# Kernel optimization log

Measured on AMD Instinct MI355X. Metric: run time of the kernel, lower is better.

## Reference

```python
import jax, jax.numpy as jnp
import numpy as np

B, N, M, C = 4, 2048, 576, 512
H, KVH, D = 8, 2, 64          # heads, kv heads, head_dim
E, TOPK, F = 8, 2, 2048       # experts, top-k, expert hidden (4*C)
EPS = 1e-6
NEG = -1e9


def setup_inputs() -> dict:
    key = jax.random.key(0)
    ks = iter(jax.random.split(key, 40))
    w = lambda shape, s=0.02: jax.random.normal(next(ks), shape, jnp.float32) * s
    d = {
        'x': jax.random.normal(next(ks), (B, N, C), jnp.float32),
        'vision_features': jax.random.normal(next(ks), (B, M, C), jnp.float32),
        'ln1_g': jnp.ones((C,), jnp.float32), 'ln1_b': jnp.zeros((C,), jnp.float32),
        'ln2_g': jnp.ones((C,), jnp.float32), 'ln2_b': jnp.zeros((C,), jnp.float32),
        'ln3_g': jnp.ones((C,), jnp.float32), 'ln3_b': jnp.zeros((C,), jnp.float32),
        # self-attention (GQA): q -> C, k/v -> KVH*D
        'sa_wq': w((C, C)), 'sa_bq': jnp.zeros((C,), jnp.float32),
        'sa_wk': w((C, KVH * D)), 'sa_bk': jnp.zeros((KVH * D,), jnp.float32),
        'sa_wv': w((C, KVH * D)), 'sa_bv': jnp.zeros((KVH * D,), jnp.float32),
        'sa_wo': w((C, C)), 'sa_bo': jnp.zeros((C,), jnp.float32),
        # cross-attention (GQA)
        'ca_wq': w((C, C)), 'ca_bq': jnp.zeros((C,), jnp.float32),
        'ca_wk': w((C, KVH * D)), 'ca_bk': jnp.zeros((KVH * D,), jnp.float32),
        'ca_wv': w((C, KVH * D)), 'ca_bv': jnp.zeros((KVH * D,), jnp.float32),
        'ca_wo': w((C, C)), 'ca_bo': jnp.zeros((C,), jnp.float32),
        # MoE: router + stacked expert MLPs (C -> F -> C, GELU)
        'router_w': w((C, E)), 'router_b': jnp.zeros((E,), jnp.float32),
        'e_w1': w((E, C, F)), 'e_b1': jnp.zeros((E, F), jnp.float32),
        'e_w2': w((E, F, C)), 'e_b2': jnp.zeros((E, C), jnp.float32),
    }
    return d


def _ln(x, g, b):
    mu = jnp.mean(x, -1, keepdims=True)
    var = jnp.mean(jnp.square(x - mu), -1, keepdims=True)
    return (x - mu) * jax.lax.rsqrt(var + EPS) * g + b


def _gqa_attn(xq, ctx, wq, bq, wk, bk, wv, bv, wo, bo, causal):
    b, n, c = xq.shape
    m = ctx.shape[1]
    q = (xq @ wq + bq).reshape(b, n, H, D).transpose(0, 2, 1, 3)      # bhnd
    k = (ctx @ wk + bk).reshape(b, m, KVH, D).transpose(0, 2, 1, 3)   # bgmd
    v = (ctx @ wv + bv).reshape(b, m, KVH, D).transpose(0, 2, 1, 3)
    rep = H // KVH
    k = jnp.repeat(k, rep, axis=1)  # repeat_interleave over head dim
    v = jnp.repeat(v, rep, axis=1)
    scores = jnp.einsum('bhnd,bhmd->bhnm', q, k) * (D ** -0.5)
    if causal:
        mask = jnp.tril(jnp.ones((n, m), bool))
        scores = jnp.where(mask, scores, NEG)
    a = jax.nn.softmax(scores, axis=-1)
    o = jnp.einsum('bhnm,bhmd->bhnd', a, v).transpose(0, 2, 1, 3).reshape(b, n, c)
    return o @ wo + bo


def _moe(x, router_w, router_b, e_w1, e_b1, e_w2, e_b2):
    logits = x @ router_w + router_b                    # [B,N,E]
    probs = jax.nn.softmax(logits, axis=-1)
    topv, topi = jax.lax.top_k(probs, TOPK)             # [B,N,K]
    topv = topv / jnp.sum(topv, -1, keepdims=True)      # renormalize top-k gates
    onehot = jax.nn.one_hot(topi, E, dtype=x.dtype)     # [B,N,K,E]
    gates = jnp.einsum('bnke,bnk->bne', onehot, topv)   # sparse gates, zeros off top-k
    h = jax.nn.gelu(jnp.einsum('bnc,ecf->bnef', x, e_w1) + e_b1)
    eo = jnp.einsum('bnef,efc->bnec', h, e_w2) + e_b2
    out = jnp.einsum('bne,bnec->bnc', gates, eo)
    # load-balance aux loss (Switch-style): E * sum_e f_e * P_e
    dispatch = jnp.sum(onehot, axis=2)                  # [B,N,E] routed mask
    f = jnp.mean(dispatch, axis=(0, 1))
    P = jnp.mean(probs, axis=(0, 1))
    aux = E * jnp.sum(f * P)
    return out, aux


def reference(x, vision_features,
              ln1_g, ln1_b, ln2_g, ln2_b, ln3_g, ln3_b,
              sa_wq, sa_bq, sa_wk, sa_bk, sa_wv, sa_bv, sa_wo, sa_bo,
              ca_wq, ca_bq, ca_wk, ca_bk, ca_wv, ca_bv, ca_wo, ca_bo,
              router_w, router_b, e_w1, e_b1, e_w2, e_b2):
    # pre-norm causal self-attn + residual
    h = _ln(x, ln1_g, ln1_b)
    x = x + _gqa_attn(h, h, sa_wq, sa_bq, sa_wk, sa_bk, sa_wv, sa_bv, sa_wo, sa_bo, True)
    # pre-norm cross-attn + residual
    h = _ln(x, ln2_g, ln2_b)
    x = x + _gqa_attn(h, vision_features, ca_wq, ca_bq, ca_wk, ca_bk, ca_wv, ca_bv, ca_wo, ca_bo, False)
    # pre-norm MoE FFN + residual
    h = _ln(x, ln3_g, ln3_b)
    m, aux = _moe(h, router_w, router_b, e_w1, e_b1, e_w2, e_b2)
    return x + m, aux
```

## Files before the change

kernel.cpp:

```cpp
#include <hip/hip_runtime.h>
#include <cstddef>
#include <cstdint>

#define B_   4
#define N_   2048
#define M_   576
#define C_   512
#define H_   8
#define KVH_ 2
#define D_   64
#define E_   8
#define F_   2048
#define BN_  (B_*N_)
#define BM_  (B_*M_)

typedef __attribute__((ext_vector_type(8))) short bf16x8;
typedef __attribute__((ext_vector_type(4))) float f32x4;

__device__ __forceinline__ unsigned short f2bf(float f) {
    union { float f; unsigned int u; } v; v.f = f;
    unsigned int r = v.u + 0x7FFFu + ((v.u >> 16) & 1u);
    return (unsigned short)(r >> 16);
}
__device__ __forceinline__ float bf2f(unsigned short u) {
    union { unsigned int u; float f; } v; v.u = ((unsigned int)u) << 16;
    return v.f;
}

typedef __attribute__((address_space(1))) void glb_void;
typedef __attribute__((address_space(3))) void lds_void;
__device__ __forceinline__ void gl2lds16(const unsigned short* g, unsigned short* l) {
    __builtin_amdgcn_global_load_lds((glb_void*)g, (lds_void*)l, 16, 0, 0);
}

__global__ __launch_bounds__(256) void prep_all(
    const float* __restrict__ sa_wq, const float* __restrict__ sa_wk,
    const float* __restrict__ sa_wv, const float* __restrict__ sa_wo,
    const float* __restrict__ ca_wq, const float* __restrict__ ca_wk,
    const float* __restrict__ ca_wv, const float* __restrict__ ca_wo,
    const float* __restrict__ e_w1, const float* __restrict__ e_w2,
    const float* __restrict__ vis,
    const float* __restrict__ sa_bk, const float* __restrict__ sa_bv,
    const float* __restrict__ ca_bk, const float* __restrict__ ca_bv,
    unsigned short* __restrict__ sa_wqt, unsigned short* __restrict__ sa_wkvt,
    unsigned short* __restrict__ sa_wot,
    unsigned short* __restrict__ ca_wqt, unsigned short* __restrict__ ca_wkvt,
    unsigned short* __restrict__ ca_wot,
    unsigned short* __restrict__ w1t, unsigned short* __restrict__ w2t,
    unsigned short* __restrict__ visbf,
    float* __restrict__ bkv_sa, float* __restrict__ bkv_ca,
    int* __restrict__ ctrl)
{
    __shared__ float T[32][33];
    int t = blockIdx.x;
    int tid = threadIdx.x;

    if (t < 17664) {
        const float* W; unsigned short* Wt; int K, N, kt, nt;
        if (t < 1280) {
            if (t < 256)      { W = sa_wq; Wt = sa_wqt; K = 512; N = 512; int r = t;        nt = r & 15; kt = r >> 4; }
            else if (t < 320) { W = sa_wk; Wt = sa_wkvt;            K = 512; N = 128; int r = t - 256; nt = r & 3;  kt = r >> 2; }
            else if (t < 384) { W = sa_wv; Wt = sa_wkvt + 128*512;  K = 512; N = 128; int r = t - 320; nt = r & 3;  kt = r >> 2; }
            else if (t < 640) { W = sa_wo; Wt = sa_wot; K = 512; N = 512; int r = t - 384;  nt = r & 15; kt = r >> 4; }
            else if (t < 896) { W = ca_wq; Wt = ca_wqt; K = 512; N = 512; int r = t - 640;  nt = r & 15; kt = r >> 4; }
            else if (t < 960) { W = ca_wk; Wt = ca_wkvt;            K = 512; N = 128; int r = t - 896; nt = r & 3;  kt = r >> 2; }
            else if (t < 1024){ W = ca_wv; Wt = ca_wkvt + 128*512;  K = 512; N = 128; int r = t - 960; nt = r & 3;  kt = r >> 2; }
            else              { W = ca_wo; Wt = ca_wot; K = 512; N = 512; int r = t - 1024; nt = r & 15; kt = r >> 4; }
        } else if (t < 9472) {
            int r = t - 1280; int e = r >> 10; r &= 1023;
            W = e_w1 + (size_t)e * C_ * F_; Wt = w1t + (size_t)e * C_ * F_;
            K = C_; N = F_; nt = r & 63; kt = r >> 6;
        } else {
            int r = t - 9472; int e = r >> 10; r &= 1023;
            W = e_w2 + (size_t)e * F_ * C_; Wt = w2t + (size_t)e * F_ * C_;
            K = F_; N = C_; nt = r & 15; kt = r >> 4;
        }
        int rr = tid >> 3, c4 = (tid & 7) * 4;
        int k0 = kt * 32, n0 = nt * 32;
        float4 v = *(const float4*)&W[(size_t)(k0 + rr) * N + n0 + c4];
        T[rr][c4 + 0] = v.x; T[rr][c4 + 1] = v.y; T[rr][c4 + 2] = v.z; T[rr][c4 + 3] = v.w;
        __syncthreads();
        ushort4 o;
        o.x = f2bf(T[c4 + 0][rr]); o.y = f2bf(T[c4 + 1][rr]);
        o.z = f2bf(T[c4 + 2][rr]); o.w = f2bf(T[c4 + 3][rr]);
        *(ushort4*)&Wt[(size_t)(n0 + rr) * K + k0 + c4] = o;
    } else if (t < 18816) {
        int i = (t - 17664) * 1024 + tid * 4;
        float4 v = *(const float4*)(vis + i);
        ushort4 o;
        o.x = f2bf(v.x); o.y = f2bf(v.y); o.z = f2bf(v.z); o.w = f2bf(v.w);
        *(ushort4*)(visbf + i) = o;
    } else {
        if (tid < 128) {
            bkv_sa[tid]       = sa_bk[tid];
            bkv_sa[128 + tid] = sa_bv[tid];
            bkv_ca[tid]       = ca_bk[tid];
            bkv_ca[128 + tid] = ca_bv[tid];
        }
        if (tid < 32) ctrl[tid] = 0;
    }
}

__global__ __launch_bounds__(256) void ln_bf(const float* __restrict__ x,
    const float* __restrict__ g, const float* __restrict__ b, unsigned short* __restrict__ out)
{
    int row = blockIdx.x;
    const float* xr = x + (size_t)row * C_;
    float s = 0.f, ss = 0.f;
    for (int c = threadIdx.x; c < C_; c += 256) { float v = xr[c]; s += v; ss += v * v; }
    __shared__ float S1[256], S2[256];
    S1[threadIdx.x] = s; S2[threadIdx.x] = ss;
    __syncthreads();
    for (int o = 128; o > 0; o >>= 1) {
        if (threadIdx.x < o) { S1[threadIdx.x] += S1[threadIdx.x + o]; S2[threadIdx.x] += S2[threadIdx.x + o]; }
        __syncthreads();
    }
    float mu  = S1[0] * (1.f / C_);
    float var = S2[0] * (1.f / C_) - mu * mu;
    float inv = rsqrtf(var + 1e-6f);
    unsigned short* orow = out + (size_t)row * C_;
    for (int c = threadIdx.x; c < C_; c += 256)
        orow[c] = f2bf((xr[c] - mu) * inv * g[c] + b[c]);
}

__global__ __launch_bounds__(256) void ln_dual(const float* __restrict__ x,
    const float* __restrict__ g, const float* __restrict__ b,
    float* __restrict__ outF, unsigned short* __restrict__ outBf)
{
    int row = blockIdx.x;
    const float* xr = x + (size_t)row * C_;
    float s = 0.f, ss = 0.f;
    for (int c = threadIdx.x; c < C_; c += 256) { float v = xr[c]; s += v; ss += v * v; }
    __shared__ float S1[256], S2[256];
    S1[threadIdx.x] = s; S2[threadIdx.x] = ss;
    __syncthreads();
    for (int o = 128; o > 0; o >>= 1) {
        if (threadIdx.x < o) { S1[threadIdx.x] += S1[threadIdx.x + o]; S2[threadIdx.x] += S2[threadIdx.x + o]; }
        __syncthreads();
    }
    float mu  = S1[0] * (1.f / C_);
    float var = S2[0] * (1.f / C_) - mu * mu;
    float inv = rsqrtf(var + 1e-6f);
    for (int c = threadIdx.x; c < C_; c += 256) {
        float v = (xr[c] - mu) * inv * g[c] + b[c];
        outF[(size_t)row * C_ + c] = v;
        outBf[(size_t)row * C_ + c] = f2bf(v);
    }
}

__global__ __launch_bounds__(256) void dense_mfma(
    const unsigned short* __restrict__ Abf,
    const unsigned short* __restrict__ Btbf,
    const float* __restrict__ bias,
    const float* __restrict__ xin,
    float* __restrict__ outF,
    unsigned short* __restrict__ outBf,
    unsigned short* __restrict__ outBf2,
    int N, int K, int mode, int NkPer)
{
    int row0 = blockIdx.y * 128;
    int col0 = blockIdx.x * 128;

    __shared__ unsigned short As[128 * 32];
    __shared__ unsigned short Bs[128 * 32];

    int tid = threadIdx.x;
    int lane = tid & 63, wid = tid >> 6;
    int lrow = lane >> 2;
    int cswz = (((lane & 3) ^ ((lane >> 3) & 3)) << 3);
    int ar0 = 16 * (wid * 2) + lrow;
    int ar1 = ar0 + 16;
    const unsigned short* gA0 = Abf + (size_t)(row0 + ar0) * K + cswz;
    const unsigned short* gA1 = Abf + (size_t)(row0 + ar1) * K + cswz;
    const unsigned short* gB0 = Btbf + (size_t)(col0 + ar0) * K + cswz;
    const unsigned short* gB1 = Btbf + (size_t)(col0 + ar1) * K + cswz;
    unsigned short* lA0 = As + (wid * 2) * 512;
    unsigned short* lA1 = lA0 + 512;
    unsigned short* lB0 = Bs + (wid * 2) * 512;
    unsigned short* lB1 = lB0 + 512;

    int wm0 = (wid & 1) * 64, wn0 = (wid >> 1) * 64;
    int lm = lane & 15, lq = lane >> 4;
    int swb = (lq ^ ((lm >> 1) & 3)) << 3;
    int aoff[4], boff[4];
#pragma unroll
    for (int i = 0; i < 4; i++) {
        aoff[i] = (wm0 + 16 * i + lm) * 32 + swb;
        boff[i] = (wn0 + 16 * i + lm) * 32 + swb;
    }

    f32x4 acc[4][4];
#pragma unroll
    for (int i = 0; i < 4; i++)
#pragma unroll
        for (int j = 0; j < 4; j++)
            acc[i][j] = (f32x4){0.f, 0.f, 0.f, 0.f};

    for (int k0 = 0; k0 < K; k0 += 32) {
        __syncthreads();
        gl2lds16(gA0 + k0, lA0);
        gl2lds16(gA1 + k0, lA1);
        gl2lds16(gB0 + k0, lB0);
        gl2lds16(gB1 + k0, lB1);
        __syncthreads();

        bf16x8 av[4], bv[4];
#pragma unroll
        for (int i = 0; i < 4; i++) av[i] = *(const bf16x8*)&As[aoff[i]];
#pragma unroll
        for (int i = 0; i < 4; i++) bv[i] = *(const bf16x8*)&Bs[boff[i]];
#pragma unroll
        for (int mi = 0; mi < 4; mi++)
#pragma unroll
            for (int ni = 0; ni < 4; ni++)
                acc[mi][ni] = __builtin_amdgcn_mfma_f32_16x16x32_bf16(av[mi], bv[ni], acc[mi][ni], 0, 0, 0);
    }

#pragma unroll
    for (int mi = 0; mi < 4; mi++) {
#pragma unroll
        for (int ri = 0; ri < 4; ri++) {
            int gr = row0 + wm0 + 16 * mi + lq * 4 + ri;
            if (mode == 3) {
#pragma unroll
                for (int ni = 0; ni < 4; ni++) {
                    int gc = col0 + wn0 + 16 * ni + lm;
                    float v = acc[mi][ni][ri] + bias[gc];
                    if (gc < 128) {
                        outBf[(size_t)gr * 128 + gc] = f2bf(v);
                    } else {
                        int bb = gr / NkPer;
                        int mm = gr - bb * NkPer;
                        outBf2[((size_t)bb * 128 + (gc - 128)) * NkPer + mm] = f2bf(v);
                    }
                }
            } else if (mode == 1) {
                size_t orow = (size_t)gr * N;
#pragma unroll
                for (int ni = 0; ni < 4; ni++) {
                    int gc = col0 + wn0 + 16 * ni + lm;
                    outF[orow + gc] += acc[mi][ni][ri] + bias[gc];
                }
            } else if (mode == 4) {
                size_t orow = (size_t)gr * N;
#pragma unroll
                for (int ni = 0; ni < 4; ni++) {
                    int gc = col0 + wn0 + 16 * ni + lm;
                    outF[orow + gc] = xin[orow + gc] + acc[mi][ni][ri] + bias[gc];
                }
            } else {
                size_t orow = (size_t)gr * N;
#pragma unroll
                for (int ni = 0; ni < 4; ni++) {
                    int gc = col0 + wn0 + 16 * ni + lm;
                    outBf[orow + gc] = f2bf(acc[mi][ni][ri] + bias[gc]);
                }
            }
        }
    }
}

__global__ __launch_bounds__(256) void attn_mfma(
    const unsigned short* __restrict__ Q,
    const unsigned short* __restrict__ K,
    const unsigned short* __restrict__ Vt,
    unsigned short* __restrict__ Obf,
    float* __restrict__ Opart,
    float* __restrict__ Lpart,
    int NkPer, int causal)
{
    __shared__ unsigned short Qs[64 * 72];
    __shared__ unsigned short Ks[64 * 72];
    __shared__ unsigned short Vs[64 * 72];
    unsigned short* Ps = Qs;

    int tid = threadIdx.x;
    int qt = blockIdx.x, bh = blockIdx.y, z = blockIdx.z;
    int b = bh >> 3, h = bh & 7, g = h >> 2;
    int q0 = qt * 64;

#pragma unroll
    for (int i = 0; i < 2; i++) {
        int s = tid + (i << 8);
        int r = s >> 3, c8 = (s & 7) << 3;
        *(uint4*)&Qs[r * 72 + c8] =
            *(const uint4*)&Q[(size_t)(b * N_ + q0 + r) * C_ + h * D_ + c8];
    }
    __syncthreads();

    int lane = tid & 63, wid = tid >> 6;
    int lm = lane & 15, lq = lane >> 4;
    int arow = wid * 16 + lm;

    bf16x8 qf[2];
    qf[0] = *(const bf16x8*)&Qs[arow * 72 + lq * 8];
    qf[1] = *(const bf16x8*)&Qs[arow * 72 + lq * 8 + 32];

    float lsum[4];
    f32x4 of[4];
#pragma unroll
    for (int i = 0; i < 4; i++) { lsum[i] = 0.f; of[i] = (f32x4){0.f,0.f,0.f,0.f}; }

    int nkt = causal ? (qt + 1) : ((NkPer + 63) >> 6);
    int nz = gridDim.z;
    int per = (nkt + nz - 1) / nz;
    int kt0 = z * per;
    int kt1 = min(nkt, kt0 + per);

    for (int kt = kt0; kt < kt1; kt++) {
        int k0 = kt << 6;
        __syncthreads();
#pragma unroll
        for (int i = 0; i < 2; i++) {
            int s = tid + (i << 8);
            int r = s >> 3, c8 = (s & 7) << 3;
            *(uint4*)&Ks[r * 72 + c8] =
                *(const uint4*)&K[(size_t)(b * NkPer + k0 + r) * (KVH_ * D_) + g * D_ + c8];
            *(uint4*)&Vs[r * 72 + c8] =
                *(const uint4*)&Vt[(size_t)(b * (KVH_ * D_) + g * D_ + r) * NkPer + k0 + c8];
        }
        __syncthreads();

        f32x4 sf[4];
#pragma unroll
        for (int i = 0; i < 4; i++) sf[i] = (f32x4){0.f,0.f,0.f,0.f};
#pragma unroll
        for (int ks = 0; ks < 2; ks++) {
#pragma unroll
            for (int ni = 0; ni < 4; ni++) {
                bf16x8 bv = *(const bf16x8*)&Ks[(16 * ni + lm) * 72 + lq * 8 + 32 * ks];
                sf[ni] = __builtin_amdgcn_mfma_f32_16x16x32_bf16(qf[ks], bv, sf[ni], 0, 0, 0);
            }
        }

        bool diag = causal && (k0 + 63 > q0 + wid * 16);
#pragma unroll
        for (int ni = 0; ni < 4; ni++)
#pragma unroll
            for (int ri = 0; ri < 4; ri++) {
                float v = sf[ni][ri] * 0.125f - 8.f;
                if (diag && (k0 + 16 * ni + lm > q0 + wid * 16 + lq * 4 + ri)) v = -1e30f;
                float p = __expf(v);
                sf[ni][ri] = p;
                lsum[ri] += p;
            }

#pragma unroll
        for (int ni = 0; ni < 4; ni++)
#pragma unroll
            for (int ri = 0; ri < 4; ri++)
                Ps[(wid * 16 + lq * 4 + ri) * 72 + 16 * ni + lm] = f2bf(sf[ni][ri]);
        __syncthreads();

        bf16x8 pf0 = *(const bf16x8*)&Ps[arow * 72 + lq * 8];
        bf16x8 pf1 = *(const bf16x8*)&Ps[arow * 72 + lq * 8 + 32];
#pragma unroll
        for (int ni = 0; ni < 4; ni++) {
            bf16x8 vv0 = *(const bf16x8*)&Vs[(16 * ni + lm) * 72 + lq * 8];
            bf16x8 vv1 = *(const bf16x8*)&Vs[(16 * ni + lm) * 72 + lq * 8 + 32];
            of[ni] = __builtin_amdgcn_mfma_f32_16x16x32_bf16(pf0, vv0, of[ni], 0, 0, 0);
            of[ni] = __builtin_amdgcn_mfma_f32_16x16x32_bf16(pf1, vv1, of[ni], 0, 0, 0);
        }
    }

#pragma unroll
    for (int ri = 0; ri < 4; ri++) {
        float s = lsum[ri];
        s += __shfl_xor(s, 1);
        s += __shfl_xor(s, 2);
        s += __shfl_xor(s, 4);
        s += __shfl_xor(s, 8);
        lsum[ri] = s;
    }

    if (nz == 1) {
#pragma unroll
        for (int ri = 0; ri < 4; ri++) {
            float inv = 1.f / lsum[ri];
            int q = q0 + wid * 16 + lq * 4 + ri;
            size_t orow = (size_t)(b * N_ + q) * C_ + h * D_;
#pragma unroll
            for (int ni = 0; ni < 4; ni++)
                Obf[orow + 16 * ni + lm] = f2bf(of[ni][ri] * inv);
        }
    } else {
        size_t zofs = (size_t)z * BN_ * C_;
#pragma unroll
        for (int ri = 0; ri < 4; ri++) {
            int q = q0 + wid * 16 + lq * 4 + ri;
            size_t orow = zofs + (size_t)(b * N_ + q) * C_ + h * D_;
#pragma unroll
            for (int ni = 0; ni < 4; ni++)
                Opart[orow + 16 * ni + lm] = of[ni][ri];
            if (lm == 0)
                Lpart[(size_t)z * (B_ * H_ * N_) + bh * N_ + q] = lsum[ri];
        }
    }
}

__global__ __launch_bounds__(256) void attn_combine(const float* __restrict__ Opart,
    const float* __restrict__ Lpart, unsigned short* __restrict__ Obf)
{
    int flat = (blockIdx.x * 256 + threadIdx.x) * 4;
    int row = flat >> 9, col = flat & 511;
    int b = row >> 11, q = row & (N_ - 1), h = col >> 6;
    int bh = b * 8 + h;
    float l = Lpart[bh * N_ + q] + Lpart[B_ * H_ * N_ + bh * N_ + q];
    float inv = 1.f / l;
    float4 o0 = *(const float4*)&Opart[flat];
    float4 o1 = *(const float4*)&Opart[(size_t)BN_ * C_ + flat];
    ushort4 o;
    o.x = f2bf((o0.x + o1.x) * inv); o.y = f2bf((o0.y + o1.y) * inv);
    o.z = f2bf((o0.z + o1.z) * inv); o.w = f2bf((o0.w + o1.w) * inv);
    *(ushort4*)&Obf[flat] = o;
}

__global__ __launch_bounds__(256) void router_logits(const float* __restrict__ X,
    const float* __restrict__ RW, const float* __restrict__ RB,
    float* __restrict__ gprobs, int* __restrict__ topi, float* __restrict__ gatesv)
{
    int lane = threadIdx.x & 63;
    int t = blockIdx.x * 4 + (threadIdx.x >> 6);
    const float* xr = X + (size_t)t * C_;
    float p[8] = {};
    for (int i = 0; i < 8; i++) {
        int c = i * 64 + lane;
        float xv = xr[c];
#pragma unroll
        for (int e = 0; e < 8; e++) p[e] = fmaf(xv, RW[c * 8 + e], p[e]);
    }
#pragma unroll
    for (int e = 0; e < 8; e++) {
        float v = p[e];
        v += __shfl_xor(v, 32, 64);
        v += __shfl_xor(v, 16, 64);
        v += __shfl_xor(v, 8, 64);
        v += __shfl_xor(v, 4, 64);
        v += __shfl_xor(v, 2, 64);
        v += __shfl_xor(v, 1, 64);
        p[e] = v;
    }
    if (lane == 0) {
        float logits[8], mx = -1e30f;
        for (int e = 0; e < 8; e++) { logits[e] = p[e] + RB[e]; mx = fmaxf(mx, logits[e]); }
        float pr[8], sum = 0.f;
        for (int e = 0; e < 8; e++) { pr[e] = expf(logits[e] - mx); sum += pr[e]; }
        float inv = 1.f / sum;
        for (int e = 0; e < 8; e++) { pr[e] *= inv; gprobs[t * 8 + e] = pr[e]; }
        int i1 = 0;
        for (int e = 1; e < 8; e++) if (pr[e] > pr[i1]) i1 = e;
        int i2 = (i1 == 0) ? 1 : 0;
        for (int e = 0; e < 8; e++) if (e != i1 && pr[e] > pr[i2]) i2 = e;
        float v1 = pr[i1], v2 = pr[i2], sg = 1.f / (v1 + v2);
        topi[t * 2]     = i1;  topi[t * 2 + 1]   = i2;
        gatesv[t * 2]   = v1 * sg;  gatesv[t * 2 + 1] = v2 * sg;
    }
}

__global__ __launch_bounds__(256) void router_reduce(const float* __restrict__ gprobs,
    const int* __restrict__ topi, int* __restrict__ ctrl, float* __restrict__ psum)
{
    __shared__ float fs[256];
    __shared__ int   is_[256];
    int bid = blockIdx.x, tid = threadIdx.x;
    if (bid < 8) {
        float s = 0.f;
        for (int t = tid; t < BN_; t += 256) s += gprobs[t * 8 + bid];
        fs[tid] = s; __syncthreads();
        for (int o = 128; o > 0; o >>= 1) { if (tid < o) fs[tid] += fs[tid + o]; __syncthreads(); }
        if (tid == 0) psum[bid] = fs[0];
    } else {
        int e = bid - 8, c = 0;
        for (int i = tid; i < BN_ * 2; i += 256) c += (topi[i] == e);
        is_[tid] = c; __syncthreads();
        for (int o = 128; o > 0; o >>= 1) { if (tid < o) is_[tid] += is_[tid + o]; __syncthreads(); }
        if (tid == 0) ctrl[e] = is_[0];
    }
}

__global__ void router_offsets(int* __restrict__ ctrl)
{
    if (threadIdx.x == 0 && blockIdx.x == 0) {
        int off = 0;
        for (int e = 0; e < 8; e++) {
            ctrl[16 + e] = off;
            off += (ctrl[e] + 127) & ~127;
        }
        ctrl[24] = off;
    }
}

__global__ __launch_bounds__(256) void router_scatter(const int* __restrict__ topi,
    const float* __restrict__ gatesv, int* __restrict__ rowtok,
    int* __restrict__ slotidx, int* __restrict__ ctrl)
{
    __shared__ int lcnt[8];
    __shared__ int lbase[8];
    int tid = threadIdx.x;
    int t = blockIdx.x * 256 + tid;
    if (tid < 8) lcnt[tid] = 0;
    __syncthreads();
    int e0 = topi[t * 2], e1 = topi[t * 2 + 1];
    int p0 = atomicAdd(&lcnt[e0], 1);
    int p1 = atomicAdd(&lcnt[e1], 1);
    __syncthreads();
    if (tid < 8) lbase[tid] = atomicAdd(&ctrl[8 + tid], lcnt[tid]);
    __syncthreads();
    int s0 = ctrl[16 + e0] + lbase[e0] + p0;
    int s1 = ctrl[16 + e1] + lbase[e1] + p1;
    rowtok[s0] = t;
    rowtok[s1] = t;
    slotidx[t * 2]     = s0;
    slotidx[t * 2 + 1] = s1;
}

__global__ __launch_bounds__(256) void moe_mfma(
    const unsigned short* __restrict__ Abf,
    const unsigned short* __restrict__ Btbf,
    const float* __restrict__ biasAll,
    unsigned short* __restrict__ outBf,
    const int* __restrict__ rowtok,
    const int* __restrict__ ctrl,
    int N, int K, int mode)
{
    int e = blockIdx.z;
    int cnt = ctrl[e];
    int row0 = blockIdx.y * 128;
    if (row0 >= cnt) return;
    int off = ctrl[16 + e];
    int col0 = blockIdx.x * 128;
    const unsigned short* Bt = Btbf + (size_t)e * N * K;
    const float* bias = biasAll + (size_t)e * N;

    __shared__ unsigned short As[128 * 64];
    __shared__ unsigned short Bs[128 * 64];
    __shared__ int toks[128];

    int tid = threadIdx.x;
    if (mode == 1 && tid < 128) {
        int gl = row0 + tid;
        toks[tid] = rowtok[off + (gl < cnt ? gl : 0)];
    }
    __syncthreads();

    int lane = tid & 63, wid = tid >> 6;
    int r8 = lane >> 3;
    size_t asrc[4], bsrc[4];
    unsigned short *adst[4], *bdst[4];
#pragma unroll
    for (int i = 0; i < 4; i++) {
        int rA = wid * 32 + i * 8 + r8;
        int srcc = (((lane & 7) ^ (rA & 7)) << 3);
        size_t arow = (mode == 1) ? (size_t)toks[rA] * K
                                  : (size_t)(off + row0 + rA) * K;
        asrc[i] = arow + srcc;
        bsrc[i] = (size_t)(col0 + rA) * K + srcc;
        adst[i] = As + (wid * 32 + i * 8) * 64;
        bdst[i] = Bs + (wid * 32 + i * 8) * 64;
    }

    int wm0 = (wid & 1) * 64, wn0 = (wid >> 1) * 64;
    int lm = lane & 15, lq = lane >> 4;
    int x7 = lm & 7;
    int aoff[4][2], boff[4][2];
#pragma unroll
    for (int i = 0; i < 4; i++) {
#pragma unroll
        for (int ks = 0; ks < 2; ks++) {
            int swz = (((ks << 2) + lq) ^ x7) << 3;
            aoff[i][ks] = (wm0 + 16 * i + lm) * 64 + swz;
            boff[i][ks] = (wn0 + 16 * i + lm) * 64 + swz;
        }
    }

    f32x4 acc[4][4];
#pragma unroll
    for (int i = 0; i < 4; i++)
#pragma unroll
        for (int j = 0; j < 4; j++)
            acc[i][j] = (f32x4){0.f, 0.f, 0.f, 0.f};

    for (int k0 = 0; k0 < K; k0 += 64) {
        __syncthreads();
#pragma unroll
        for (int i = 0; i < 4; i++) {
            gl2lds16(Abf + asrc[i] + k0, adst[i]);
            gl2lds16(Bt  + bsrc[i] + k0, bdst[i]);
        }
        __syncthreads();

#pragma unroll
        for (int ks = 0; ks < 2; ks++) {
            bf16x8 av[4], bv[4];
#pragma unroll
            for (int i = 0; i < 4; i++) av[i] = *(const bf16x8*)&As[aoff[i][ks]];
#pragma unroll
            for (int i = 0; i < 4; i++) bv[i] = *(const bf16x8*)&Bs[boff[i][ks]];
#pragma unroll
            for (int mi = 0; mi < 4; mi++)
#pragma unroll
                for (int ni = 0; ni < 4; ni++)
                    acc[mi][ni] = __builtin_amdgcn_mfma_f32_16x16x32_bf16(av[mi], bv[ni], acc[mi][ni], 0, 0, 0);
        }
    }

#pragma unroll
    for (int mi = 0; mi < 4; mi++) {
#pragma unroll
        for (int ri = 0; ri < 4; ri++) {
            int gl = row0 + wm0 + 16 * mi + lq * 4 + ri;
            size_t orow = (size_t)(off + gl) * N;
            if (mode == 1) {
#pragma unroll
                for (int ni = 0; ni < 4; ni++) {
                    int gc = col0 + wn0 + 16 * ni + lm;
                    float hv = 0.f;
                    if (gl < cnt) {
                        float xv = acc[mi][ni][ri] + bias[gc];
                        float z = 0.7978845608f * xv * fmaf(0.044715f, xv * xv, 1.f);
                        hv = __fdividef(xv, 1.f + __expf(-2.f * z));
                    }
                    outBf[orow + gc] = f2bf(hv);
                }
            } else {
#pragma unroll
                for (int ni = 0; ni < 4; ni++) {
                    int gc = col0 + wn0 + 16 * ni + lm;
                    outBf[orow + gc] = f2bf(acc[mi][ni][ri] + bias[gc]);
                }
            }
        }
    }
}

__global__ __launch_bounds__(256) void moe_combine(const unsigned short* __restrict__ slots,
    const int* __restrict__ slotidx, const float* __restrict__ gatesv,
    float* __restrict__ out)
{
    int flat = (blockIdx.x * 256 + threadIdx.x) * 4;
    int t = flat >> 9, c = flat & 511;
    int s0 = slotidx[t * 2], s1 = slotidx[t * 2 + 1];
    float g0 = gatesv[t * 2], g1 = gatesv[t * 2 + 1];
    ushort4 a = *(const ushort4*)&slots[(size_t)s0 * C_ + c];
    ushort4 b = *(const ushort4*)&slots[(size_t)s1 * C_ + c];
    float4 o = *(float4*)&out[flat];
    o.x += g0 * bf2f(a.x) + g1 * bf2f(b.x);
    o.y += g0 * bf2f(a.y) + g1 * bf2f(b.y);
    o.z += g0 * bf2f(a.z) + g1 * bf2f(b.z);
    o.w += g0 * bf2f(a.w) + g1 * bf2f(b.w);
    *(float4*)&out[flat] = o;
}

__global__ void aux_kernel(const int* __restrict__ ctrl, const float* __restrict__ psum,
                           float* __restrict__ outaux)
{
    if (threadIdx.x == 0 && blockIdx.x == 0) {
        float s = 0.f;
        for (int e = 0; e < 8; e++)
            s += ((float)ctrl[e] / (float)BN_) * (psum[e] / (float)BN_);
        outaux[0] = 8.f * s;
    }
}

extern "C" void kernel_launch(void* const* d_in, const int* in_sizes, int n_in,
                              void* d_out, int out_size, void* d_ws, size_t ws_size,
                              hipStream_t stream)
{
    const float* x      = (const float*)d_in[0];
    const float* vis    = (const float*)d_in[1];
    const float* ln1g   = (const float*)d_in[2];
    const float* ln1b   = (const float*)d_in[3];
    const float* ln2g   = (const float*)d_in[4];
    const float* ln2b   = (const float*)d_in[5];
    const float* ln3g   = (const float*)d_in[6];
    const float* ln3b   = (const float*)d_in[7];
    const float* sa_wq  = (const float*)d_in[8];
    const float* sa_bq  = (const float*)d_in[9];
    const float* sa_wk  = (const float*)d_in[10];
    const float* sa_bk  = (const float*)d_in[11];
    const float* sa_wv  = (const float*)d_in[12];
    const float* sa_bv  = (const float*)d_in[13];
    const float* sa_wo  = (const float*)d_in[14];
    const float* sa_bo  = (const float*)d_in[15];
    const float* ca_wq  = (const float*)d_in[16];
    const float* ca_bq  = (const float*)d_in[17];
    const float* ca_wk  = (const float*)d_in[18];
    const float* ca_bk  = (const float*)d_in[19];
    const float* ca_wv  = (const float*)d_in[20];
    const float* ca_bv  = (const float*)d_in[21];
    const float* ca_wo  = (const float*)d_in[22];
    const float* ca_bo  = (const float*)d_in[23];
    const float* rw     = (const float*)d_in[24];
    const float* rb     = (const float*)d_in[25];
    const float* e_w1   = (const float*)d_in[26];
    const float* e_b1   = (const float*)d_in[27];
    const float* e_w2   = (const float*)d_in[28];
    const float* e_b2   = (const float*)d_in[29];

    float* out = (float*)d_out;

    char* ws = (char*)d_ws;
    size_t off = 0;
    auto alloc = [&](size_t bytes) -> void* {
        void* p = ws + off;
        off = (off + bytes + 255) & ~(size_t)255;
        return p;
    };
    float* hbuf    = (float*)alloc((size_t)BN_ * C_ * 4);
    unsigned short* hbz = (unsigned short*)alloc((size_t)BN_ * C_ * 2);
    unsigned short* visbf = (unsigned short*)alloc((size_t)BM_ * C_ * 2);
    unsigned short* eoslots = (unsigned short*)hbuf;
    char* ureg = (char*)alloc((size_t)17408 * F_ * 2);
    unsigned short* moeH = (unsigned short*)ureg;
    unsigned short* qbf  = (unsigned short*)(ureg);
    unsigned short* obf  = (unsigned short*)(ureg + (size_t)BN_ * C_ * 2);
    unsigned short* kbf  = (unsigned short*)(ureg + (size_t)BN_ * C_ * 4);
    unsigned short* vtbf = (unsigned short*)(ureg + (size_t)BN_ * C_ * 4 + (size_t)BN_ * KVH_ * D_ * 2);
    float* opart = (float*)(ureg + (size_t)BN_ * C_ * 4 + (size_t)BN_ * KVH_ * D_ * 4);
    float* lpart = (float*)(ureg + (size_t)BN_ * C_ * 4 + (size_t)BN_ * KVH_ * D_ * 4
                                 + (size_t)2 * BN_ * C_ * 4);
    unsigned short* sa_wqt = (unsigned short*)alloc((size_t)C_ * C_ * 2);
    unsigned short* sa_wkvt = (unsigned short*)alloc((size_t)C_ * 2 * KVH_ * D_ * 2);
    unsigned short* sa_wot = (unsigned short*)alloc((size_t)C_ * C_ * 2);
    unsigned short* ca_wqt = (unsigned short*)alloc((size_t)C_ * C_ * 2);
    unsigned short* ca_wkvt = (unsigned short*)alloc((size_t)C_ * 2 * KVH_ * D_ * 2);
    unsigned short* ca_wot = (unsigned short*)alloc((size_t)C_ * C_ * 2);
    float* bkv_sa = (float*)alloc(256 * 4);
    float* bkv_ca = (float*)alloc(256 * 4);
    unsigned short* w1t  = (unsigned short*)alloc((size_t)E_ * C_ * F_ * 2);
    unsigned short* w2t  = (unsigned short*)alloc((size_t)E_ * F_ * C_ * 2);
    float* gprobs  = (float*)alloc((size_t)BN_ * 8 * 4);
    int*   topi    = (int*)  alloc((size_t)BN_ * 2 * 4);
    float* gatesv  = (float*)alloc((size_t)BN_ * 2 * 4);
    int*   rowtok  = (int*)  alloc(17408 * 4);
    int*   slotidx = (int*)  alloc((size_t)BN_ * 2 * 4);
    int*   ctrl    = (int*)  alloc(256);
    float* psum    = (float*)((char*)ctrl + 128);
    (void)ws_size; (void)in_sizes; (void)n_in; (void)out_size;

    prep_all<<<18817, 256, 0, stream>>>(
        sa_wq, sa_wk, sa_wv, sa_wo, ca_wq, ca_wk, ca_wv, ca_wo,
        e_w1, e_w2, vis, sa_bk, sa_bv, ca_bk, ca_bv,
        sa_wqt, sa_wkvt, sa_wot, ca_wqt, ca_wkvt, ca_wot,
        w1t, w2t, visbf, bkv_sa, bkv_ca, ctrl);

    ln_bf<<<BN_, 256, 0, stream>>>(x, ln1g, ln1b, hbz);
    dense_mfma<<<dim3(4, 64), 256, 0, stream>>>(hbz, sa_wqt, sa_bq, nullptr, nullptr, qbf, nullptr, C_, C_, 0, 0);
    dense_mfma<<<dim3(2, 64), 256, 0, stream>>>(hbz, sa_wkvt, bkv_sa, nullptr, nullptr, kbf, vtbf, 256, C_, 3, N_);
    attn_mfma<<<dim3(N_/64, B_*H_, 2), 256, 0, stream>>>(qbf, kbf, vtbf, nullptr, opart, lpart, N_, 1);
    attn_combine<<<(BN_*C_)/1024, 256, 0, stream>>>(opart, lpart, obf);
    dense_mfma<<<dim3(4, 64), 256, 0, stream>>>(obf, sa_wot, sa_bo, x, out, nullptr, nullptr, C_, C_, 4, 0);

    ln_bf<<<BN_, 256, 0, stream>>>(out, ln2g, ln2b, hbz);
    dense_mfma<<<dim3(4, 64), 256, 0, stream>>>(hbz, ca_wqt, ca_bq, nullptr, nullptr, qbf, nullptr, C_, C_, 0, 0);
    dense_mfma<<<dim3(2, 18), 256, 0, stream>>>(visbf, ca_wkvt, bkv_ca, nullptr, nullptr, kbf, vtbf, 256, C_, 3, M_);
    attn_mfma<<<dim3(N_/64, B_*H_, 1), 256, 0, stream>>>(qbf, kbf, vtbf, obf, nullptr, nullptr, M_, 0);
    dense_mfma<<<dim3(4, 64), 256, 0, stream>>>(obf, ca_wot, ca_bo, nullptr, out, nullptr, nullptr, C_, C_, 1, 0);

    ln_dual<<<BN_, 256, 0, stream>>>(out, ln3g, ln3b, hbuf, hbz);
    router_logits<<<BN_/4, 256, 0, stream>>>(hbuf, rw, rb, gprobs, topi, gatesv);
    router_reduce<<<16, 256, 0, stream>>>(gprobs, topi, ctrl, psum);
    router_offsets<<<1, 1, 0, stream>>>(ctrl);
    router_scatter<<<BN_/256, 256, 0, stream>>>(topi, gatesv, rowtok, slotidx, ctrl);
    moe_mfma<<<dim3(F_/128, BN_/128, E_), 256, 0, stream>>>(
        hbz, w1t, e_b1, moeH, rowtok, ctrl, F_, C_, 1);
    moe_mfma<<<dim3(C_/128, BN_/128, E_), 256, 0, stream>>>(
        moeH, w2t, e_b2, eoslots, rowtok, ctrl, C_, F_, 2);
    moe_combine<<<(BN_*C_)/1024, 256, 0, stream>>>(eoslots, slotidx, gatesv, out);
    aux_kernel<<<1, 1, 0, stream>>>(ctrl, psum, out + (size_t)BN_ * C_);
}
```

Measured before the change: 660.1 us.

## Fuse self-attn QKV projection, widen attention splits, fold tiny control kernels

Merges the self-attention Q and K/V projections into one GEMM with a new epilogue (mode 5). That epilogue writes Q, K and the transposed V, and it relies on the K/V weights sitting right after the Q weights in memory. Self-attention now uses three key splits instead of two, and cross-attention uses two splits plus a generic combine kernel. This is meant to raise parallelism, at the cost of extra partial-result traffic through memory. The router offset computation moves into router_reduce through a last-block atomic counter, and the aux-loss kernel is folded into moe_combine, which removes two single-thread launches.

```diff
diff --git a/kernel.cpp b/kernel.cpp
--- a/kernel.cpp
+++ b/kernel.cpp
@@ -40,6 +40,7 @@
     const float* __restrict__ ca_wv, const float* __restrict__ ca_wo,
     const float* __restrict__ e_w1, const float* __restrict__ e_w2,
     const float* __restrict__ vis,
+    const float* __restrict__ sa_bq,
     const float* __restrict__ sa_bk, const float* __restrict__ sa_bv,
     const float* __restrict__ ca_bk, const float* __restrict__ ca_bv,
     unsigned short* __restrict__ sa_wqt, unsigned short* __restrict__ sa_wkvt,
@@ -48,7 +49,7 @@
     unsigned short* __restrict__ ca_wot,
     unsigned short* __restrict__ w1t, unsigned short* __restrict__ w2t,
     unsigned short* __restrict__ visbf,
-    float* __restrict__ bkv_sa, float* __restrict__ bkv_ca,
+    float* __restrict__ bqkv_sa, float* __restrict__ bkv_ca,
     int* __restrict__ ctrl)
 {
     __shared__ float T[32][33];
@@ -91,11 +92,12 @@
         o.x = f2bf(v.x); o.y = f2bf(v.y); o.z = f2bf(v.z); o.w = f2bf(v.w);
         *(ushort4*)(visbf + i) = o;
     } else {
+        for (int c = tid; c < 512; c += 256) bqkv_sa[c] = sa_bq[c];
         if (tid < 128) {
-            bkv_sa[tid]       = sa_bk[tid];
-            bkv_sa[128 + tid] = sa_bv[tid];
-            bkv_ca[tid]       = ca_bk[tid];
-            bkv_ca[128 + tid] = ca_bv[tid];
+            bqkv_sa[512 + tid] = sa_bk[tid];
+            bqkv_sa[640 + tid] = sa_bv[tid];
+            bkv_ca[tid]        = ca_bk[tid];
+            bkv_ca[128 + tid]  = ca_bv[tid];
         }
         if (tid < 32) ctrl[tid] = 0;
     }
@@ -156,6 +158,7 @@
     float* __restrict__ outF,
     unsigned short* __restrict__ outBf,
     unsigned short* __restrict__ outBf2,
+    unsigned short* __restrict__ outBf3,
     int N, int K, int mode, int NkPer)
 {
     int row0 = blockIdx.y * 128;
@@ -221,7 +224,22 @@
 #pragma unroll
         for (int ri = 0; ri < 4; ri++) {
             int gr = row0 + wm0 + 16 * mi + lq * 4 + ri;
-            if (mode == 3) {
+            if (mode == 5) {
+#pragma unroll
+                for (int ni = 0; ni < 4; ni++) {
+                    int gc = col0 + wn0 + 16 * ni + lm;
+                    float v = acc[mi][ni][ri] + bias[gc];
+                    if (gc < 512) {
+                        outBf[(size_t)gr * 512 + gc] = f2bf(v);
+                    } else if (gc < 640) {
+                        outBf2[(size_t)gr * 128 + (gc - 512)] = f2bf(v);
+                    } else {
+                        int bb = gr / NkPer;
+                        int mm = gr - bb * NkPer;
+                        outBf3[((size_t)bb * 128 + (gc - 640)) * NkPer + mm] = f2bf(v);
+                    }
+                }
+            } else if (mode == 3) {
 #pragma unroll
                 for (int ni = 0; ni < 4; ni++) {
                     int gc = col0 + wn0 + 16 * ni + lm;
@@ -264,7 +282,6 @@
     const unsigned short* __restrict__ Q,
     const unsigned short* __restrict__ K,
     const unsigned short* __restrict__ Vt,
-    unsigned short* __restrict__ Obf,
     float* __restrict__ Opart,
     float* __restrict__ Lpart,
     int NkPer, int causal)
@@ -373,46 +390,38 @@
         lsum[ri] = s;
     }
 
-    if (nz == 1) {
-#pragma unroll
-        for (int ri = 0; ri < 4; ri++) {
-            float inv = 1.f / lsum[ri];
-            int q = q0 + wid * 16 + lq * 4 + ri;
-            size_t orow = (size_t)(b * N_ + q) * C_ + h * D_;
-#pragma unroll
-            for (int ni = 0; ni < 4; ni++)
-                Obf[orow + 16 * ni + lm] = f2bf(of[ni][ri] * inv);
-        }
-    } else {
-        size_t zofs = (size_t)z * BN_ * C_;
-#pragma unroll
-        for (int ri = 0; ri < 4; ri++) {
-            int q = q0 + wid * 16 + lq * 4 + ri;
-            size_t orow = zofs + (size_t)(b * N_ + q) * C_ + h * D_;
-#pragma unroll
-            for (int ni = 0; ni < 4; ni++)
-                Opart[orow + 16 * ni + lm] = of[ni][ri];
-            if (lm == 0)
-                Lpart[(size_t)z * (B_ * H_ * N_) + bh * N_ + q] = lsum[ri];
-        }
+    size_t zofs = (size_t)z * BN_ * C_;
+#pragma unroll
+    for (int ri = 0; ri < 4; ri++) {
+        int q = q0 + wid * 16 + lq * 4 + ri;
+        size_t orow = zofs + (size_t)(b * N_ + q) * C_ + h * D_;
+#pragma unroll
+        for (int ni = 0; ni < 4; ni++)
+            Opart[orow + 16 * ni + lm] = of[ni][ri];
+        if (lm == 0)
+            Lpart[(size_t)z * (B_ * H_ * N_) + bh * N_ + q] = lsum[ri];
     }
 }
 
 __global__ __launch_bounds__(256) void attn_combine(const float* __restrict__ Opart,
-    const float* __restrict__ Lpart, unsigned short* __restrict__ Obf)
+    const float* __restrict__ Lpart, unsigned short* __restrict__ Obf, int Z)
 {
     int flat = (blockIdx.x * 256 + threadIdx.x) * 4;
     int row = flat >> 9, col = flat & 511;
     int b = row >> 11, q = row & (N_ - 1), h = col >> 6;
     int bh = b * 8 + h;
-    float l = Lpart[bh * N_ + q] + Lpart[B_ * H_ * N_ + bh * N_ + q];
+    float l = 0.f;
+    for (int z = 0; z < Z; z++) l += Lpart[(size_t)z * (B_ * H_ * N_) + bh * N_ + q];
+    float4 o = {0.f, 0.f, 0.f, 0.f};
+    for (int z = 0; z < Z; z++) {
+        float4 oz = *(const float4*)&Opart[(size_t)z * BN_ * C_ + flat];
+        o.x += oz.x; o.y += oz.y; o.z += oz.z; o.w += oz.w;
+    }
     float inv = 1.f / l;
-    float4 o0 = *(const float4*)&Opart[flat];
-    float4 o1 = *(const float4*)&Opart[(size_t)BN_ * C_ + flat];
-    ushort4 o;
-    o.x = f2bf((o0.x + o1.x) * inv); o.y = f2bf((o0.y + o1.y) * inv);
-    o.z = f2bf((o0.z + o1.z) * inv); o.w = f2bf((o0.w + o1.w) * inv);
-    *(ushort4*)&Obf[flat] = o;
+    ushort4 ob;
+    ob.x = f2bf(o.x * inv); ob.y = f2bf(o.y * inv);
+    ob.z = f2bf(o.z * inv); ob.w = f2bf(o.w * inv);
+    *(ushort4*)&Obf[flat] = ob;
 }
 
 __global__ __launch_bounds__(256) void router_logits(const float* __restrict__ X,
@@ -476,17 +485,18 @@
         for (int o = 128; o > 0; o >>= 1) { if (tid < o) is_[tid] += is_[tid + o]; __syncthreads(); }
         if (tid == 0) ctrl[e] = is_[0];
     }
-}
-
-__global__ void router_offsets(int* __restrict__ ctrl)
-{
-    if (threadIdx.x == 0 && blockIdx.x == 0) {
-        int off = 0;
-        for (int e = 0; e < 8; e++) {
-            ctrl[16 + e] = off;
-            off += (ctrl[e] + 127) & ~127;
-        }
-        ctrl[24] = off;
+    if (tid == 0) {
+        __threadfence();
+        int done = atomicAdd(&ctrl[25], 1);
+        if (done == 15) {
+            __threadfence();
+            int off = 0;
+            for (int e = 0; e < 8; e++) {
+                ctrl[16 + e] = off;
+                off += (ctrl[e] + 127) & ~127;
+            }
+            ctrl[24] = off;
+        }
     }
 }
 
@@ -635,6 +645,7 @@
 
 __global__ __launch_bounds__(256) void moe_combine(const unsigned short* __restrict__ slots,
     const int* __restrict__ slotidx, const float* __restrict__ gatesv,
+    const int* __restrict__ ctrl, const float* __restrict__ psum,
     float* __restrict__ out)
 {
     int flat = (blockIdx.x * 256 + threadIdx.x) * 4;
@@ -649,16 +660,11 @@
     o.z += g0 * bf2f(a.z) + g1 * bf2f(b.z);
     o.w += g0 * bf2f(a.w) + g1 * bf2f(b.w);
     *(float4*)&out[flat] = o;
-}
-
-__global__ void aux_kernel(const int* __restrict__ ctrl, const float* __restrict__ psum,
-                           float* __restrict__ outaux)
-{
-    if (threadIdx.x == 0 && blockIdx.x == 0) {
+    if (blockIdx.x == 0 && threadIdx.x == 0) {
         float s = 0.f;
         for (int e = 0; e < 8; e++)
             s += ((float)ctrl[e] / (float)BN_) * (psum[e] / (float)BN_);
-        outaux[0] = 8.f * s;
+        out[(size_t)BN_ * C_] = 8.f * s;
     }
 }
 
@@ -717,16 +723,15 @@
     unsigned short* kbf  = (unsigned short*)(ureg + (size_t)BN_ * C_ * 4);
     unsigned short* vtbf = (unsigned short*)(ureg + (size_t)BN_ * C_ * 4 + (size_t)BN_ * KVH_ * D_ * 2);
     float* opart = (float*)(ureg + (size_t)BN_ * C_ * 4 + (size_t)BN_ * KVH_ * D_ * 4);
-    float* lpart = (float*)(ureg + (size_t)BN_ * C_ * 4 + (size_t)BN_ * KVH_ * D_ * 4
-                                 + (size_t)2 * BN_ * C_ * 4);
+    float* lpart = (float*)alloc((size_t)3 * B_ * H_ * N_ * 4);
     unsigned short* sa_wqt = (unsigned short*)alloc((size_t)C_ * C_ * 2);
     unsigned short* sa_wkvt = (unsigned short*)alloc((size_t)C_ * 2 * KVH_ * D_ * 2);
     unsigned short* sa_wot = (unsigned short*)alloc((size_t)C_ * C_ * 2);
     unsigned short* ca_wqt = (unsigned short*)alloc((size_t)C_ * C_ * 2);
     unsigned short* ca_wkvt = (unsigned short*)alloc((size_t)C_ * 2 * KVH_ * D_ * 2);
     unsigned short* ca_wot = (unsigned short*)alloc((size_t)C_ * C_ * 2);
-    float* bkv_sa = (float*)alloc(256 * 4);
-    float* bkv_ca = (float*)alloc(256 * 4);
+    float* bqkv_sa = (float*)alloc(768 * 4);
+    float* bkv_ca  = (float*)alloc(256 * 4);
     unsigned short* w1t  = (unsigned short*)alloc((size_t)E_ * C_ * F_ * 2);
     unsigned short* w2t  = (unsigned short*)alloc((size_t)E_ * F_ * C_ * 2);
     float* gprobs  = (float*)alloc((size_t)BN_ * 8 * 4);
@@ -740,32 +745,35 @@
 
     prep_all<<<18817, 256, 0, stream>>>(
         sa_wq, sa_wk, sa_wv, sa_wo, ca_wq, ca_wk, ca_wv, ca_wo,
-        e_w1, e_w2, vis, sa_bk, sa_bv, ca_bk, ca_bv,
+        e_w1, e_w2, vis, sa_bq, sa_bk, sa_bv, ca_bk, ca_bv,
         sa_wqt, sa_wkvt, sa_wot, ca_wqt, ca_wkvt, ca_wot,
-        w1t, w2t, visbf, bkv_sa, bkv_ca, ctrl);
+        w1t, w2t, visbf, bqkv_sa, bkv_ca, ctrl);
 
     ln_bf<<<BN_, 256, 0, stream>>>(x, ln1g, ln1b, hbz);
-    dense_mfma<<<dim3(4, 64), 256, 0, stream>>>(hbz, sa_wqt, sa_bq, nullptr, nullptr, qbf, nullptr, C_, C_, 0, 0);
-    dense_mfma<<<dim3(2, 64), 256, 0, stream>>>(hbz, sa_wkvt, bkv_sa, nullptr, nullptr, kbf, vtbf, 256, C_, 3, N_);
-    attn_mfma<<<dim3(N_/64, B_*H_, 2), 256, 0, stream>>>(qbf, kbf, vtbf, nullptr, opart, lpart, N_, 1);
-    attn_combine<<<(BN_*C_)/1024, 256, 0, stream>>>(opart, lpart, obf);
-    dense_mfma<<<dim3(4, 64), 256, 0, stream>>>(obf, sa_wot, sa_bo, x, out, nullptr, nullptr, C_, C_, 4, 0);
+    dense_mfma<<<dim3(6, 64), 256, 0, stream>>>(hbz, sa_wqt, bqkv_sa, nullptr, nullptr,
+                                                qbf, kbf, vtbf, 768, C_, 5, N_);
+    attn_mfma<<<dim3(N_/64, B_*H_, 3), 256, 0, stream>>>(qbf, kbf, vtbf, opart, lpart, N_, 1);
+    attn_combine<<<(BN_*C_)/1024, 256, 0, stream>>>(opart, lpart, obf, 3);
+    dense_mfma<<<dim3(4, 64), 256, 0, stream>>>(obf, sa_wot, sa_bo, x, out,
+                                                nullptr, nullptr, nullptr, C_, C_, 4, 0);
 
     ln_bf<<<BN_, 256, 0, stream>>>(out, ln2g, ln2b, hbz);
-    dense_mfma<<<dim3(4, 64), 256, 0, stream>>>(hbz, ca_wqt, ca_bq, nullptr, nullptr, qbf, nullptr, C_, C_, 0, 0);
-    dense_mfma<<<dim3(2, 18), 256, 0, stream>>>(visbf, ca_wkvt, bkv_ca, nullptr, nullptr, kbf, vtbf, 256, C_, 3, M_);
-    attn_mfma<<<dim3(N_/64, B_*H_, 1), 256, 0, stream>>>(qbf, kbf, vtbf, obf, nullptr, nullptr, M_, 0);
-    dense_mfma<<<dim3(4, 64), 256, 0, stream>>>(obf, ca_wot, ca_bo, nullptr, out, nullptr, nullptr, C_, C_, 1, 0);
+    dense_mfma<<<dim3(4, 64), 256, 0, stream>>>(hbz, ca_wqt, ca_bq, nullptr, nullptr,
+                                                qbf, nullptr, nullptr, C_, C_, 0, 0);
+    dense_mfma<<<dim3(2, 18), 256, 0, stream>>>(visbf, ca_wkvt, bkv_ca, nullptr, nullptr,
+                                                kbf, vtbf, nullptr, 256, C_, 3, M_);
+    attn_mfma<<<dim3(N_/64, B_*H_, 2), 256, 0, stream>>>(qbf, kbf, vtbf, opart, lpart, M_, 0);
+    attn_combine<<<(BN_*C_)/1024, 256, 0, stream>>>(opart, lpart, obf, 2);
+    dense_mfma<<<dim3(4, 64), 256, 0, stream>>>(obf, ca_wot, ca_bo, nullptr, out,
+                                                nullptr, nullptr, nullptr, C_, C_, 1, 0);
 
     ln_dual<<<BN_, 256, 0, stream>>>(out, ln3g, ln3b, hbuf, hbz);
     router_logits<<<BN_/4, 256, 0, stream>>>(hbuf, rw, rb, gprobs, topi, gatesv);
     router_reduce<<<16, 256, 0, stream>>>(gprobs, topi, ctrl, psum);
-    router_offsets<<<1, 1, 0, stream>>>(ctrl);
     router_scatter<<<BN_/256, 256, 0, stream>>>(topi, gatesv, rowtok, slotidx, ctrl);
     moe_mfma<<<dim3(F_/128, BN_/128, E_), 256, 0, stream>>>(
         hbz, w1t, e_b1, moeH, rowtok, ctrl, F_, C_, 1);
     moe_mfma<<<dim3(C_/128, BN_/128, E_), 256, 0, stream>>>(
         moeH, w2t, e_b2, eoslots, rowtok, ctrl, C_, F_, 2);
-    moe_combine<<<(BN_*C_)/1024, 256, 0, stream>>>(eoslots, slotidx, gatesv, out);
-    aux_kernel<<<1, 1, 0, stream>>>(ctrl, psum, out + (size_t)BN_ * C_);
-}
+    moe_combine<<<(BN_*C_)/1024, 256, 0, stream>>>(eoslots, slotidx, gatesv, ctrl, psum, out);
+}
```

Measured after the change: 650.0 us. Within noise of the previous version (-1.5%).
